# Kernel optimization log

Measured on AMD Instinct MI355X. Metric: run time of the kernel, lower is better.

Reference implementation:

```python
import jax, jax.numpy as jnp
import numpy as np
import math

NUM_HEADS = 16
SIZE = 1024
HEAD_SIZE = SIZE // NUM_HEADS
B, S = 2, 2048


def setup_inputs() -> dict:
    key = jax.random.key(0)
    ks = jax.random.split(key, 11)
    sc = 1.0 / math.sqrt(SIZE)
    inp = {
        "q": jax.random.normal(ks[0], (B, S, SIZE), dtype=jnp.float32),
        "k": jax.random.normal(ks[1], (B, S, SIZE), dtype=jnp.float32),
        "v": jax.random.normal(ks[2], (B, S, SIZE), dtype=jnp.float32),
        "Wq": jax.random.normal(ks[3], (SIZE, SIZE), dtype=jnp.float32) * sc,
        "bq": jax.random.normal(ks[4], (SIZE,), dtype=jnp.float32) * sc,
        "Wk": jax.random.normal(ks[5], (SIZE, SIZE), dtype=jnp.float32) * sc,
        "bk": jax.random.normal(ks[6], (SIZE,), dtype=jnp.float32) * sc,
        "Wv": jax.random.normal(ks[7], (SIZE, SIZE), dtype=jnp.float32) * sc,
        "bv": jax.random.normal(ks[8], (SIZE,), dtype=jnp.float32) * sc,
        "Wo": jax.random.normal(ks[9], (SIZE, SIZE), dtype=jnp.float32) * sc,
        "bo": jax.random.normal(ks[10], (SIZE,), dtype=jnp.float32) * sc,
    }
    return inp


def _split_heads(x):
    # [B, S, SIZE] -> [B, H, S, D]
    b, s, _ = x.shape
    return x.reshape(b, s, NUM_HEADS, HEAD_SIZE).transpose(0, 2, 1, 3)


def reference(q, k, v, Wq, bq, Wk, bk, Wv, bv, Wo, bo):
    qh = _split_heads(q @ Wq.T + bq) / math.sqrt(HEAD_SIZE)  # [B,H,S,D]
    kh = _split_heads(k @ Wk.T + bk)
    vh = _split_heads(v @ Wv.T + bv)
    scores = jnp.einsum("bhqd,bhkd->bhqk", qh, kh)  # [B,H,S,S]
    attn = jax.nn.softmax(scores, axis=-1)
    ctx = jnp.einsum("bhqk,bhkd->bhqd", attn, vh)  # [B,H,S,D]
    ctx = ctx.transpose(0, 2, 1, 3).reshape(q.shape[0], -1, SIZE)
    return ctx @ Wo.T + bo
```

## Files before the change

kernel.cpp:

```cpp
#include <hip/hip_runtime.h>
#include <hip/hip_bf16.h>

#define SIZE 1024
#define NH 16
#define HD 64
#define BB 2
#define SS 2048
#define MROWS (BB * SS)
#define QT 256
#define NQT (SS / QT)
#define NKT ((SS / 2) / 64)

using bf16 = __hip_bfloat16;
using frag16 = __attribute__((ext_vector_type(8))) short;
using f32x4 = __attribute__((ext_vector_type(4))) float;
using f32x16 = __attribute__((ext_vector_type(16))) float;
typedef unsigned int u32;
typedef __attribute__((ext_vector_type(4))) unsigned int u32x4v;

__device__ __forceinline__ void glds16(const bf16* g, bf16* l) {
    __builtin_amdgcn_global_load_lds(
        (const __attribute__((address_space(1))) u32*)g,
        (__attribute__((address_space(3))) u32*)l, 16, 0, 0);
}

__device__ __forceinline__ void cvt_store8(bf16* dst, const float* src) {
    float4 a = *(const float4*)src;
    float4 b = *(const float4*)(src + 4);
    bf16 t[8];
    t[0] = __float2bfloat16(a.x); t[1] = __float2bfloat16(a.y);
    t[2] = __float2bfloat16(a.z); t[3] = __float2bfloat16(a.w);
    t[4] = __float2bfloat16(b.x); t[5] = __float2bfloat16(b.y);
    t[6] = __float2bfloat16(b.z); t[7] = __float2bfloat16(b.w);
    *(uint4*)dst = *(const uint4*)t;
}

__global__ __launch_bounds__(256) void cast_kernel(
    const float* __restrict__ Wq, const float* __restrict__ Wk,
    const float* __restrict__ Wv, const float* __restrict__ Wo,
    const float* __restrict__ q, const float* __restrict__ k,
    const float* __restrict__ v,
    bf16* __restrict__ Wb, bf16* __restrict__ qb,
    bf16* __restrict__ kb, bf16* __restrict__ vb)
{
    const size_t WN = (size_t)SIZE * SIZE;
    const size_t AN = (size_t)MROWS * SIZE;
    const size_t e = ((size_t)blockIdx.x * 256 + threadIdx.x) * 8;
    if (e < 4 * WN) {
        const int which = (int)(e >> 20);
        const size_t off = e & (WN - 1);
        const float* s = (which == 0) ? Wq : (which == 1) ? Wk : (which == 2) ? Wv : Wo;
        cvt_store8(Wb + e, s + off);
    } else {
        const size_t a = e - 4 * WN;
        const int which = (int)(a >> 22);
        const size_t off = a & (AN - 1);
        const float* s = (which == 0) ? q : (which == 1) ? k : v;
        bf16* d = (which == 0) ? qb : (which == 1) ? kb : vb;
        cvt_store8(d + off, s + off);
    }
}

__device__ __forceinline__ void gemm_body(
    const bf16* __restrict__ X, const bf16* __restrict__ W,
    const float* __restrict__ bias, bf16* __restrict__ Y, float scale, bool vt_mode,
    int bm, int bn)
{
    __shared__ __align__(16) bf16 smem[16384];
    bf16* As = smem;
    bf16* Bs = smem + 8192;

    const int tid = threadIdx.x;
    const int wave = tid >> 6;
    const int lane = tid & 63;
    const int lane15 = lane & 15;
    const int quad = lane >> 4;
    const int wm = (wave & 1) * 64;
    const int wn = (wave >> 1) * 64;

    f32x4 acc[4][4];
#pragma unroll
    for (int i = 0; i < 4; i++)
#pragma unroll
        for (int j = 0; j < 4; j++)
            acc[i][j] = (f32x4){0.f, 0.f, 0.f, 0.f};

    const int srow = lane >> 2;
    const int scol = (lane & 3) * 8;

#define STAGE(KT, BUF)                                                         \
    {                                                                          \
        _Pragma("unroll")                                                      \
        for (int n = 0; n < 2; n++) {                                          \
            const int c = wave * 2 + n;          \
            glds16(X + (size_t)(bm + c * 16 + srow) * SIZE + (KT) * 32 + scol, \
                   As + (BUF) * 4096 + c * 512);                               \
            glds16(W + (size_t)(bn + c * 16 + srow) * SIZE + (KT) * 32 + scol, \
                   Bs + (BUF) * 4096 + c * 512);                               \
        }                                                                      \
    }

    STAGE(0, 0);
    __syncthreads();

    for (int kt = 0; kt < SIZE / 32; kt++) {
        const int buf = kt & 1;
        if (kt + 1 < SIZE / 32) STAGE(kt + 1, buf ^ 1);
        __builtin_amdgcn_sched_barrier(0);

        frag16 a[4], b[4];
#pragma unroll
        for (int mi = 0; mi < 4; mi++)
            a[mi] = *(const frag16*)(As + buf * 4096 + (wm + mi * 16 + lane15) * 32 + quad * 8);
#pragma unroll
        for (int ni = 0; ni < 4; ni++)
            b[ni] = *(const frag16*)(Bs + buf * 4096 + (wn + ni * 16 + lane15) * 32 + quad * 8);
#pragma unroll
        for (int mi = 0; mi < 4; mi++)
#pragma unroll
            for (int ni = 0; ni < 4; ni++)
                acc[mi][ni] = __builtin_amdgcn_mfma_f32_16x16x32_bf16(
                    a[mi], b[ni], acc[mi][ni], 0, 0, 0);

        __syncthreads();
    }
#undef STAGE

    if (!vt_mode) {
#pragma unroll
        for (int ni = 0; ni < 4; ni++) {
            const int col = bn + wn + ni * 16 + lane15;
            const float bv = bias[col];
#pragma unroll
            for (int mi = 0; mi < 4; mi++) {
                const int row = bm + wm + mi * 16 + quad * 4;
#pragma unroll
                for (int r = 0; r < 4; r++)
                    Y[(size_t)(row + r) * SIZE + col] =
                        __float2bfloat16((acc[mi][ni][r] + bv) * scale);
            }
        }
    } else {
        bf16* tr = smem;
        const int bloc = bm >> 11;
        const int s0g = bm & (SS - 1);
#pragma unroll
        for (int p = 0; p < 2; p++) {
            __syncthreads();
            if ((wave >> 1) == p) {
#pragma unroll
                for (int ni = 0; ni < 4; ni++) {
                    const int colp = ni * 16 + lane15;
                    const float bv = bias[bn + p * 64 + colp];
#pragma unroll
                    for (int mi = 0; mi < 4; mi++) {
                        const int row = wm + mi * 16 + quad * 4;
#pragma unroll
                        for (int r = 0; r < 4; r++)
                            tr[colp * 136 + row + r] =
                                __float2bfloat16(acc[mi][ni][r] + bv);
                    }
                }
            }
            __syncthreads();
            const int colp = tid >> 2;
            const int gcol = bn + p * 64 + colp;
            const int hh = gcol >> 6, dd = gcol & (HD - 1);
            bf16* dst = (bf16*)Y + ((size_t)(bloc * NH + hh) * HD + dd) * SS
                        + s0g + (tid & 3) * 32;
            const bf16* src = tr + colp * 136 + (tid & 3) * 32;
#pragma unroll
            for (int j = 0; j < 4; j++)
                *(uint4*)(dst + j * 8) = *(const uint4*)(src + j * 8);
        }
    }
}

__global__ __launch_bounds__(256) void qkv_proj_kernel(
    const bf16* __restrict__ qb, const bf16* __restrict__ kb, const bf16* __restrict__ vb,
    const bf16* __restrict__ Wb,
    const float* __restrict__ bq, const float* __restrict__ bk, const float* __restrict__ bv,
    bf16* __restrict__ qh, bf16* __restrict__ kh, bf16* __restrict__ vt)
{
    const int f = blockIdx.x;
    const int w = (f & 7) * 96 + (f >> 3);
    const int z = w >> 8;
    const int rem = w & 255;
    const int bn = (rem & 7) * 128;
    const int bm = (rem >> 3) * 128;

    const bf16 *X, *W; const float* bi; bf16* Y; float sc; bool vm;
    if (z == 0)      { X = qb; W = Wb;                   bi = bq; Y = qh; sc = 0.125f; vm = false; }
    else if (z == 1) { X = kb; W = Wb + SIZE * SIZE;     bi = bk; Y = kh; sc = 1.0f;   vm = false; }
    else             { X = vb; W = Wb + 2 * SIZE * SIZE; bi = bv; Y = vt; sc = 1.0f;   vm = true;  }
    gemm_body(X, W, bi, Y, sc, vm, bm, bn);
}

__global__ __launch_bounds__(256) void attn_kernel(
    const bf16* __restrict__ qh, const bf16* __restrict__ kh,
    const bf16* __restrict__ vt, bf16* __restrict__ po, float* __restrict__ pl)
{
    __shared__ __align__(16) bf16 Ks[2][64][72];
    __shared__ __align__(16) bf16 Vs[2][64][72];

    const int tid = threadIdx.x;
    const int wave = tid >> 6;
    const int lane = tid & 63;
    const int L31 = lane & 31;
    const int t8 = (lane >> 5) * 8;

    const int f = blockIdx.x;
    const int w = (f & 7) * 64 + (f >> 3);
    const int bh = w >> 4;
    const int within = w & 15;
    const int b = bh >> 4;
    const int h = bh & 15;
    const int qt = within >> 1;
    const int sh = within & 1;
    const int q0 = qt * QT;

    const size_t baseq = (size_t)b * SS * SIZE + (size_t)h * HD;
    const size_t basev = (size_t)(b * NH + h) * HD * SS;
    const float LOG2E = 1.44269504088896340736f;
    const float OFF = 12.0f * LOG2E;

    frag16 aq[2][4];
#pragma unroll
    for (int m2 = 0; m2 < 2; m2++) {
        const bf16* qp = qh + baseq
            + (size_t)(q0 + wave * 64 + m2 * 32 + L31) * SIZE + t8;
#pragma unroll
        for (int kk = 0; kk < 4; kk++)
            aq[m2][kk] = *(const frag16*)(qp + kk * 16);
    }

    f32x16 ofrag[2][2];
#pragma unroll
    for (int m2 = 0; m2 < 2; m2++)
#pragma unroll
        for (int d2 = 0; d2 < 2; d2++)
#pragma unroll
            for (int r = 0; r < 16; r++)
                ofrag[m2][d2][r] = 0.f;
    float lsc[2] = {0.f, 0.f};

    const int sr = tid >> 3;
    const int sc = (tid & 7) * 8;

    uint4 rk0, rk1, rv0, rv1;
#define ISSUE(KT)                                                              \
    {                                                                          \
        const int s0_ = sh * (SS / 2) + (KT) * 64;                             \
        rk0 = *(const uint4*)(kh + baseq + (size_t)(s0_ + sr) * SIZE + sc);    \
        rk1 = *(const uint4*)(kh + baseq + (size_t)(s0_ + sr + 32) * SIZE + sc);\
        rv0 = *(const uint4*)(vt + basev + (size_t)sr * SS + s0_ + sc);        \
        rv1 = *(const uint4*)(vt + basev + (size_t)(sr + 32) * SS + s0_ + sc); \
    }
#define COMMIT(BUF)                                                            \
    {                                                                          \
        *(uint4*)&Ks[BUF][sr][sc] = rk0; *(uint4*)&Ks[BUF][sr + 32][sc] = rk1; \
        *(uint4*)&Vs[BUF][sr][sc] = rv0; *(uint4*)&Vs[BUF][sr + 32][sc] = rv1; \
    }

    ISSUE(0); COMMIT(0);
    __syncthreads();

    for (int kt = 0; kt < NKT; kt++) {
        const int buf = kt & 1;
        if (kt + 1 < NKT) ISSUE(kt + 1);
        __builtin_amdgcn_sched_barrier(0);

#pragma unroll
        for (int n2 = 0; n2 < 2; n2++) {
            frag16 kfr[4];
#pragma unroll
            for (int kk = 0; kk < 4; kk++)
                kfr[kk] = *(const frag16*)&Ks[buf][n2 * 32 + L31][kk * 16 + t8];

            frag16 pa[2][2];
#pragma unroll
            for (int m2 = 0; m2 < 2; m2++) {
                f32x16 c;
#pragma unroll
                for (int r = 0; r < 16; r++) c[r] = 0.f;
#pragma unroll
                for (int kk = 0; kk < 4; kk++)
                    c = __builtin_amdgcn_mfma_f32_32x32x16_bf16(
                        kfr[kk], aq[m2][kk], c, 0, 0, 0);
                float p[16];
                float s = 0.f;
#pragma unroll
                for (int r = 0; r < 16; r++) {
                    p[r] = exp2f(c[r] * LOG2E - OFF);
                    s += p[r];
                }
                lsc[m2] += s;
                u32 wv[4][2];
#pragma unroll
                for (int s4 = 0; s4 < 4; s4++)
#pragma unroll
                    for (int j = 0; j < 2; j++)
                        asm("v_cvt_pk_bf16_f32 %0, %1, %2"
                            : "=v"(wv[s4][j])
                            : "v"(p[s4 * 4 + 2 * j]), "v"(p[s4 * 4 + 2 * j + 1]));
#pragma unroll
                for (int kk2 = 0; kk2 < 2; kk2++) {
                    u32x4v wd;
#pragma unroll
                    for (int j = 0; j < 2; j++) {
                        auto rr = __builtin_amdgcn_permlane32_swap(
                            wv[2 * kk2][j], wv[2 * kk2 + 1][j], false, false);
                        wd[j] = rr[0];
                        wd[2 + j] = rr[1];
                    }
                    pa[m2][kk2] = __builtin_bit_cast(frag16, wd);
                }
            }

            __builtin_amdgcn_s_setprio(1);
#pragma unroll
            for (int kk2 = 0; kk2 < 2; kk2++)
#pragma unroll
                for (int d2 = 0; d2 < 2; d2++) {
                    frag16 vfr = *(const frag16*)
                        &Vs[buf][d2 * 32 + L31][n2 * 32 + kk2 * 16 + t8];
#pragma unroll
                    for (int m2 = 0; m2 < 2; m2++)
                        ofrag[m2][d2] = __builtin_amdgcn_mfma_f32_32x32x16_bf16(
                            pa[m2][kk2], vfr, ofrag[m2][d2], 0, 0, 0);
                }
            __builtin_amdgcn_s_setprio(0);
        }

        if (kt + 1 < NKT) {
            COMMIT(buf ^ 1);
            __syncthreads();
        }
    }
#undef ISSUE
#undef COMMIT

    const int pb = ((b * NH + h) * NQT + qt) * 2 + sh;
    {
        float* plp = pl + (size_t)pb * QT;
#pragma unroll
        for (int m2 = 0; m2 < 2; m2++) {
            const float ltot = lsc[m2] + __shfl_xor(lsc[m2], 32);
            if (lane < 32)
                plp[wave * 64 + m2 * 32 + L31] = ltot;
        }
    }
    bf16* pop = po + (size_t)pb * QT * HD;
    const int t4 = (lane >> 5) * 4;
#pragma unroll
    for (int m2 = 0; m2 < 2; m2++)
#pragma unroll
        for (int d2 = 0; d2 < 2; d2++)
#pragma unroll
            for (int r = 0; r < 16; r++) {
                const int row = wave * 64 + m2 * 32 + (r & 3) + 8 * (r >> 2) + t4;
                pop[(size_t)row * HD + d2 * 32 + L31] =
                    __float2bfloat16(ofrag[m2][d2][r]);
            }
}

__global__ __launch_bounds__(256) void out_proj_kernel(
    const bf16* __restrict__ po, const float* __restrict__ pl,
    const bf16* __restrict__ Wob, const float* __restrict__ bo,
    float* __restrict__ out)
{
    __shared__ __align__(16) bf16 As[2 * 64 * 32];
    __shared__ __align__(16) bf16 Bs[2 * 128 * 32];

    const int f = blockIdx.x;
    const int w = (f & 7) * 64 + (f >> 3);
    const int bn = (w & 7) * 128;
    const int bm = (w >> 3) * 64;

    const int tid = threadIdx.x;
    const int wave = tid >> 6;
    const int lane = tid & 63;
    const int lane15 = lane & 15;
    const int quad = lane >> 4;
    const int wn = wave * 32;

    f32x4 acc[4][2];
#pragma unroll
    for (int i = 0; i < 4; i++)
#pragma unroll
        for (int j = 0; j < 2; j++)
            acc[i][j] = (f32x4){0.f, 0.f, 0.f, 0.f};

    const int srow = lane >> 2;
    const int scol = (lane & 3) * 8;

    const int arow = tid >> 2;
    const int acol = (tid & 3) * 8;
    const int gr = bm + arow;
    const int bIdx = gr >> 11;
    const int s = gr & (SS - 1);
    const int qt8 = s >> 8;
    const int sq = s & (QT - 1);

    uint4 p0a, p1a, p0b, p1b;
    float l0, l1;

#define ALOAD(KT)                                                                 \
    {                                                                             \
        const int pb0_ = ((bIdx * NH + (KT)) * NQT + qt8) * 2;                    \
        const bf16* q0_ = po + (size_t)pb0_ * QT * HD + sq * HD;                  \
        const bf16* q1_ = po + (size_t)(pb0_ + 1) * QT * HD + sq * HD;            \
        p0a = *(const uint4*)(q0_ + acol);                                        \
        p0b = *(const uint4*)(q0_ + 32 + acol);                                   \
        p1a = *(const uint4*)(q1_ + acol);                                        \
        p1b = *(const uint4*)(q1_ + 32 + acol);                                   \
        l0 = pl[(size_t)pb0_ * QT + sq];                                          \
        l1 = pl[(size_t)(pb0_ + 1) * QT + sq];                                    \
    }

    ALOAD(0);

    for (int kt = 0; kt < NH; kt++) {
        __syncthreads();
        {
            const float inv = 1.0f / fmaxf(l0 + l1, 1e-30f);
            const bf16* x0 = (const bf16*)&p0a; const bf16* y0 = (const bf16*)&p1a;
            const bf16* x1 = (const bf16*)&p0b; const bf16* y1 = (const bf16*)&p1b;
            bf16 o0[8], o1[8];
#pragma unroll
            for (int e = 0; e < 8; e++) {
                o0[e] = __float2bfloat16((__bfloat162float(x0[e]) + __bfloat162float(y0[e])) * inv);
                o1[e] = __float2bfloat16((__bfloat162float(x1[e]) + __bfloat162float(y1[e])) * inv);
            }
            *(uint4*)(As + 0 * 2048 + arow * 32 + acol) = *(const uint4*)o0;
            *(uint4*)(As + 1 * 2048 + arow * 32 + acol) = *(const uint4*)o1;
        }
#pragma unroll
        for (int n = 0; n < 4; n++) {
            const int c = wave * 4 + n;
            const int plane = c >> 3;
            const int cc = c & 7;
            glds16(Wob + (size_t)(bn + cc * 16 + srow) * SIZE + kt * 64 + plane * 32 + scol,
                   Bs + c * 512);
        }
        __syncthreads();

        if (kt + 1 < NH) ALOAD(kt + 1);

#pragma unroll
        for (int kk = 0; kk < 2; kk++) {
            frag16 a[4], b[2];
#pragma unroll
            for (int mi = 0; mi < 4; mi++)
                a[mi] = *(const frag16*)(As + kk * 2048 + (mi * 16 + lane15) * 32 + quad * 8);
#pragma unroll
            for (int ni = 0; ni < 2; ni++)
                b[ni] = *(const frag16*)(Bs + kk * 4096 + (wn + ni * 16 + lane15) * 32 + quad * 8);
#pragma unroll
            for (int mi = 0; mi < 4; mi++)
#pragma unroll
                for (int ni = 0; ni < 2; ni++)
                    acc[mi][ni] = __builtin_amdgcn_mfma_f32_16x16x32_bf16(
                        a[mi], b[ni], acc[mi][ni], 0, 0, 0);
        }
    }
#undef ALOAD

#pragma unroll
    for (int ni = 0; ni < 2; ni++) {
        const int col = bn + wn + ni * 16 + lane15;
        const float bv = bo[col];
#pragma unroll
        for (int mi = 0; mi < 4; mi++) {
            const int row = bm + mi * 16 + quad * 4;
#pragma unroll
            for (int r = 0; r < 4; r++)
                out[(size_t)(row + r) * SIZE + col] = acc[mi][ni][r] + bv;
        }
    }
}

extern "C" void kernel_launch(void* const* d_in, const int* in_sizes, int n_in,
                              void* d_out, int out_size, void* d_ws, size_t ws_size,
                              hipStream_t stream) {
    const float* q  = (const float*)d_in[0];
    const float* k  = (const float*)d_in[1];
    const float* v  = (const float*)d_in[2];
    const float* Wq = (const float*)d_in[3];
    const float* bq = (const float*)d_in[4];
    const float* Wk = (const float*)d_in[5];
    const float* bk = (const float*)d_in[6];
    const float* Wv = (const float*)d_in[7];
    const float* bv = (const float*)d_in[8];
    const float* Wo = (const float*)d_in[9];
    const float* bo = (const float*)d_in[10];
    float* out = (float*)d_out;

    bf16* Wb  = (bf16*)d_ws;
    bf16* qb  = Wb + (size_t)4 * SIZE * SIZE;
    bf16* kb  = qb + (size_t)MROWS * SIZE;
    bf16* vb  = kb + (size_t)MROWS * SIZE;
    bf16* qh  = vb + (size_t)MROWS * SIZE;
    bf16* kh  = qh + (size_t)MROWS * SIZE;
    bf16* vt  = kh + (size_t)MROWS * SIZE;
    bf16* po  = qb;
    float* pl = (float*)Wb;

    cast_kernel<<<dim3(8192, 1, 1), 256, 0, stream>>>(
        Wq, Wk, Wv, Wo, q, k, v, Wb, qb, kb, vb);
    qkv_proj_kernel<<<dim3(768, 1, 1), 256, 0, stream>>>(
        qb, kb, vb, Wb, bq, bk, bv, qh, kh, vt);
    attn_kernel<<<dim3(512, 1, 1), 256, 0, stream>>>(qh, kh, vt, po, pl);
    out_proj_kernel<<<dim3(512, 1, 1), 256, 0, stream>>>(
        po, pl, Wb + (size_t)3 * SIZE * SIZE, bo, out);
}
```

Baseline: 248.0 us.

## Halve attention query tile to 128 rows, doubling blocks and occupancy

Shrinks the attention query tile from 256 to 128 rows so each wave handles 32 query rows instead of 64. This doubles the grid to 1024 blocks, and launch_bounds now requests 4 blocks per CU, both aimed at better latency hiding and load balance. The out-projection indexing is updated to the new partial-result layout. In exchange, each K/V tile loaded into LDS is reused by half as many query rows, so LDS and global K/V traffic per FLOP roughly doubles.

Result: no change. 244.2 us (-1.5%).

```diff
diff --git a/kernel.cpp b/kernel.cpp
--- a/kernel.cpp
+++ b/kernel.cpp
@@ -7,7 +7,7 @@
 #define BB 2
 #define SS 2048
 #define MROWS (BB * SS)
-#define QT 256
+#define QT 128
 #define NQT (SS / QT)
 #define NKT ((SS / 2) / 64)
 
@@ -196,7 +196,7 @@
     gemm_body(X, W, bi, Y, sc, vm, bm, bn);
 }
 
-__global__ __launch_bounds__(256) void attn_kernel(
+__global__ __launch_bounds__(256, 4) void attn_kernel(
     const bf16* __restrict__ qh, const bf16* __restrict__ kh,
     const bf16* __restrict__ vt, bf16* __restrict__ po, float* __restrict__ pl)
 {
@@ -210,9 +210,9 @@
     const int t8 = (lane >> 5) * 8;
 
     const int f = blockIdx.x;
-    const int w = (f & 7) * 64 + (f >> 3);
-    const int bh = w >> 4;
-    const int within = w & 15;
+    const int w = (f & 7) * 128 + (f >> 3);
+    const int bh = w >> 5;
+    const int within = w & 31;
     const int b = bh >> 4;
     const int h = bh & 15;
     const int qt = within >> 1;
@@ -224,25 +224,21 @@
     const float LOG2E = 1.44269504088896340736f;
     const float OFF = 12.0f * LOG2E;
 
-    frag16 aq[2][4];
-#pragma unroll
-    for (int m2 = 0; m2 < 2; m2++) {
-        const bf16* qp = qh + baseq
-            + (size_t)(q0 + wave * 64 + m2 * 32 + L31) * SIZE + t8;
+    frag16 aq[4];
+    {
+        const bf16* qp = qh + baseq + (size_t)(q0 + wave * 32 + L31) * SIZE + t8;
 #pragma unroll
         for (int kk = 0; kk < 4; kk++)
-            aq[m2][kk] = *(const frag16*)(qp + kk * 16);
-    }
-
-    f32x16 ofrag[2][2];
-#pragma unroll
-    for (int m2 = 0; m2 < 2; m2++)
-#pragma unroll
-        for (int d2 = 0; d2 < 2; d2++)
-#pragma unroll
-            for (int r = 0; r < 16; r++)
-                ofrag[m2][d2][r] = 0.f;
-    float lsc[2] = {0.f, 0.f};
+            aq[kk] = *(const frag16*)(qp + kk * 16);
+    }
+
+    f32x16 ofrag[2];
+#pragma unroll
+    for (int d2 = 0; d2 < 2; d2++)
+#pragma unroll
+        for (int r = 0; r < 16; r++)
+            ofrag[d2][r] = 0.f;
+    float lsc = 0.f;
 
     const int sr = tid >> 3;
     const int sc = (tid & 7) * 8;
@@ -277,44 +273,41 @@
             for (int kk = 0; kk < 4; kk++)
                 kfr[kk] = *(const frag16*)&Ks[buf][n2 * 32 + L31][kk * 16 + t8];
 
-            frag16 pa[2][2];
-#pragma unroll
-            for (int m2 = 0; m2 < 2; m2++) {
-                f32x16 c;
-#pragma unroll
-                for (int r = 0; r < 16; r++) c[r] = 0.f;
-#pragma unroll
-                for (int kk = 0; kk < 4; kk++)
-                    c = __builtin_amdgcn_mfma_f32_32x32x16_bf16(
-                        kfr[kk], aq[m2][kk], c, 0, 0, 0);
-                float p[16];
-                float s = 0.f;
-#pragma unroll
-                for (int r = 0; r < 16; r++) {
-                    p[r] = exp2f(c[r] * LOG2E - OFF);
-                    s += p[r];
+            f32x16 c;
+#pragma unroll
+            for (int r = 0; r < 16; r++) c[r] = 0.f;
+#pragma unroll
+            for (int kk = 0; kk < 4; kk++)
+                c = __builtin_amdgcn_mfma_f32_32x32x16_bf16(
+                    kfr[kk], aq[kk], c, 0, 0, 0);
+            float p[16];
+            float s = 0.f;
+#pragma unroll
+            for (int r = 0; r < 16; r++) {
+                p[r] = exp2f(c[r] * LOG2E - OFF);
+                s += p[r];
+            }
+            lsc += s;
+            u32 wv[4][2];
+#pragma unroll
+            for (int s4 = 0; s4 < 4; s4++)
+#pragma unroll
+                for (int j = 0; j < 2; j++)
+                    asm("v_cvt_pk_bf16_f32 %0, %1, %2"
+                        : "=v"(wv[s4][j])
+                        : "v"(p[s4 * 4 + 2 * j]), "v"(p[s4 * 4 + 2 * j + 1]));
+            frag16 pa[2];
+#pragma unroll
+            for (int kk2 = 0; kk2 < 2; kk2++) {
+                u32x4v wd;
+#pragma unroll
+                for (int j = 0; j < 2; j++) {
+                    auto rr = __builtin_amdgcn_permlane32_swap(
+                        wv[2 * kk2][j], wv[2 * kk2 + 1][j], false, false);
+                    wd[j] = rr[0];
+                    wd[2 + j] = rr[1];
                 }
-                lsc[m2] += s;
-                u32 wv[4][2];
-#pragma unroll
-                for (int s4 = 0; s4 < 4; s4++)
-#pragma unroll
-                    for (int j = 0; j < 2; j++)
-                        asm("v_cvt_pk_bf16_f32 %0, %1, %2"
-                            : "=v"(wv[s4][j])
-                            : "v"(p[s4 * 4 + 2 * j]), "v"(p[s4 * 4 + 2 * j + 1]));
-#pragma unroll
-                for (int kk2 = 0; kk2 < 2; kk2++) {
-                    u32x4v wd;
-#pragma unroll
-                    for (int j = 0; j < 2; j++) {
-                        auto rr = __builtin_amdgcn_permlane32_swap(
-                            wv[2 * kk2][j], wv[2 * kk2 + 1][j], false, false);
-                        wd[j] = rr[0];
-                        wd[2 + j] = rr[1];
-                    }
-                    pa[m2][kk2] = __builtin_bit_cast(frag16, wd);
-                }
+                pa[kk2] = __builtin_bit_cast(frag16, wd);
             }
 
             __builtin_amdgcn_s_setprio(1);
@@ -324,10 +317,8 @@
                 for (int d2 = 0; d2 < 2; d2++) {
                     frag16 vfr = *(const frag16*)
                         &Vs[buf][d2 * 32 + L31][n2 * 32 + kk2 * 16 + t8];
-#pragma unroll
-                    for (int m2 = 0; m2 < 2; m2++)
-                        ofrag[m2][d2] = __builtin_amdgcn_mfma_f32_32x32x16_bf16(
-                            pa[m2][kk2], vfr, ofrag[m2][d2], 0, 0, 0);
+                    ofrag[d2] = __builtin_amdgcn_mfma_f32_32x32x16_bf16(
+                        pa[kk2], vfr, ofrag[d2], 0, 0, 0);
                 }
             __builtin_amdgcn_s_setprio(0);
         }
@@ -342,26 +333,20 @@
 
     const int pb = ((b * NH + h) * NQT + qt) * 2 + sh;
     {
-        float* plp = pl + (size_t)pb * QT;
-#pragma unroll
-        for (int m2 = 0; m2 < 2; m2++) {
-            const float ltot = lsc[m2] + __shfl_xor(lsc[m2], 32);
-            if (lane < 32)
-                plp[wave * 64 + m2 * 32 + L31] = ltot;
-        }
+        const float ltot = lsc + __shfl_xor(lsc, 32);
+        if (lane < 32)
+            pl[(size_t)pb * QT + wave * 32 + L31] = ltot;
     }
     bf16* pop = po + (size_t)pb * QT * HD;
     const int t4 = (lane >> 5) * 4;
 #pragma unroll
-    for (int m2 = 0; m2 < 2; m2++)
-#pragma unroll
-        for (int d2 = 0; d2 < 2; d2++)
-#pragma unroll
-            for (int r = 0; r < 16; r++) {
-                const int row = wave * 64 + m2 * 32 + (r & 3) + 8 * (r >> 2) + t4;
-                pop[(size_t)row * HD + d2 * 32 + L31] =
-                    __float2bfloat16(ofrag[m2][d2][r]);
-            }
+    for (int d2 = 0; d2 < 2; d2++)
+#pragma unroll
+        for (int r = 0; r < 16; r++) {
+            const int row = wave * 32 + (r & 3) + 8 * (r >> 2) + t4;
+            pop[(size_t)row * HD + d2 * 32 + L31] =
+                __float2bfloat16(ofrag[d2][r]);
+        }
 }
 
 __global__ __launch_bounds__(256) void out_proj_kernel(
@@ -399,7 +384,7 @@
     const int gr = bm + arow;
     const int bIdx = gr >> 11;
     const int s = gr & (SS - 1);
-    const int qt8 = s >> 8;
+    const int qt8 = s >> 7;
     const int sq = s & (QT - 1);
 
     uint4 p0a, p1a, p0b, p1b;
@@ -510,7 +495,7 @@
         Wq, Wk, Wv, Wo, q, k, v, Wb, qb, kb, vb);
     qkv_proj_kernel<<<dim3(768, 1, 1), 256, 0, stream>>>(
         qb, kb, vb, Wb, bq, bk, bv, qh, kh, vt);
-    attn_kernel<<<dim3(512, 1, 1), 256, 0, stream>>>(qh, kh, vt, po, pl);
+    attn_kernel<<<dim3(1024, 1, 1), 256, 0, stream>>>(qh, kh, vt, po, pl);
     out_proj_kernel<<<dim3(512, 1, 1), 256, 0, stream>>>(
         po, pl, Wb + (size_t)3 * SIZE * SIZE, bo, out);
 }
```
